# Kernel optimization log

Measured on AMD Instinct MI355X. Metric: run time of the kernel, lower is better.

## Reference

```python
import jax, jax.numpy as jnp
import numpy as np

V, H, L, NH, DH, FF, P, T = 21128, 768, 12, 12, 64, 3072, 512, 9
B, S = 16, 256
EPS = 1e-12

def _ln(x, g, b):
    m = x.mean(-1, keepdims=True)
    v = ((x - m) ** 2).mean(-1, keepdims=True)
    return (x - m) * jax.lax.rsqrt(v + EPS) * g + b

def setup_inputs() -> dict:
    key = jax.random.key(0)
    ks = iter(jax.random.split(key, 64))
    def nrm(shape, s=0.02):
        return (jax.random.normal(next(ks), shape, jnp.float32) * s)
    inp = {
        'input_ids': jax.random.randint(next(ks), (B, 1, S), 0, V, dtype=jnp.int32),
        'token_type_ids': jnp.zeros((B, 1, S), jnp.int32),
        'attention_mask': jnp.ones((B, 1, S), jnp.int32),
        'tags': jax.random.randint(next(ks), (B, S), 0, T, dtype=jnp.int32),
        'word_emb': nrm((V, H)), 'pos_emb': nrm((P, H)), 'type_emb': nrm((2, H)),
        'emb_ln_g': jnp.ones((H,), jnp.float32), 'emb_ln_b': jnp.zeros((H,), jnp.float32),
        'Wq': nrm((L, H, H)), 'bq': jnp.zeros((L, H), jnp.float32),
        'Wk': nrm((L, H, H)), 'bk': jnp.zeros((L, H), jnp.float32),
        'Wv': nrm((L, H, H)), 'bv': jnp.zeros((L, H), jnp.float32),
        'Wo': nrm((L, H, H)), 'bo': jnp.zeros((L, H), jnp.float32),
        'ln1_g': jnp.ones((L, H), jnp.float32), 'ln1_b': jnp.zeros((L, H), jnp.float32),
        'W1': nrm((L, H, FF)), 'b1': jnp.zeros((L, FF), jnp.float32),
        'W2': nrm((L, FF, H)), 'b2': jnp.zeros((L, H), jnp.float32),
        'ln2_g': jnp.ones((L, H), jnp.float32), 'ln2_b': jnp.zeros((L, H), jnp.float32),
        'dense_W': nrm((H, T)), 'dense_b': jnp.zeros((T,), jnp.float32),
        'crf_start': nrm((T,), 0.1), 'crf_end': nrm((T,), 0.1), 'crf_trans': nrm((T, T), 0.1),
    }
    return inp

def _model(input_ids, token_type_ids, attention_mask, tags,
           word_emb, pos_emb, type_emb, emb_ln_g, emb_ln_b,
           Wq, bq, Wk, bk, Wv, bv, Wo, bo, ln1_g, ln1_b,
           W1, b1, W2, b2, ln2_g, ln2_b, dense_W, dense_b,
           crf_start, crf_end, crf_trans):
    ids = input_ids[:, 0, :]            # [B,S]
    tt = token_type_ids[:, 0, :]
    amask = attention_mask[:, 0, :]     # [B,S] int
    Bn, Sn = ids.shape
    # --- BERT embeddings (post-LN BERT-base) ---
    x = word_emb[ids] + pos_emb[:Sn][None, :, :] + type_emb[tt]
    x = _ln(x, emb_ln_g, emb_ln_b)
    bias = jnp.where(amask[:, None, None, :] > 0, 0.0, -1e9).astype(x.dtype)  # [B,1,1,S]
    scale = 1.0 / np.sqrt(DH).astype(np.float32)
    def layer(h, p):
        wq, bq_, wk, bk_, wv, bv_, wo, bo_, g1, c1, w1, d1, w2, d2, g2, c2 = p
        q = (h @ wq + bq_).reshape(Bn, Sn, NH, DH).transpose(0, 2, 1, 3)
        k = (h @ wk + bk_).reshape(Bn, Sn, NH, DH).transpose(0, 2, 1, 3)
        v = (h @ wv + bv_).reshape(Bn, Sn, NH, DH).transpose(0, 2, 1, 3)
        att = jax.nn.softmax(jnp.einsum('bhqd,bhkd->bhqk', q, k) * scale + bias, axis=-1)
        ctx = jnp.einsum('bhqk,bhkd->bhqd', att, v).transpose(0, 2, 1, 3).reshape(Bn, Sn, H)
        h = _ln(h + ctx @ wo + bo_, g1, c1)
        ff = jax.nn.gelu(h @ w1 + d1, approximate=False)
        h = _ln(h + ff @ w2 + d2, g2, c2)
        return h, None
    x, _ = jax.lax.scan(layer, x, (Wq, bq, Wk, bk, Wv, bv, Wo, bo, ln1_g, ln1_b, W1, b1, W2, b2, ln2_g, ln2_b))
    # --- emission head, seq-first like the torch code ---
    emis = (x @ dense_W + dense_b).transpose(1, 0, 2)   # [S,B,T]
    m = (amask.T > 0)                                    # [S,B] bool
    tags_sb = tags.T                                     # [S,B]
    bidx = jnp.arange(Bn)
    # --- CRF numerator (gold path score) ---
    score0 = crf_start[tags_sb[0]] + emis[0, bidx, tags_sb[0]]
    def num_step(sc, inp):
        e, t, tp, mm = inp
        inc = crf_trans[tp, t] + e[bidx, t]
        return sc + jnp.where(mm, inc, 0.0), None
    score, _ = jax.lax.scan(num_step, score0, (emis[1:], tags_sb[1:], tags_sb[:-1], m[1:]))
    lengths = m.astype(jnp.int32).sum(0)                 # [B]
    last_tag = jnp.take_along_axis(tags_sb, (lengths - 1)[None, :], axis=0)[0]
    score = score + crf_end[last_tag]
    # --- CRF partition (forward algorithm) ---
    alpha0 = crf_start[None, :] + emis[0]                # [B,T]
    def fwd_step(a, inp):
        e, mm = inp
        nxt = jax.nn.logsumexp(a[:, :, None] + crf_trans[None, :, :] + e[:, None, :], axis=1)
        return jnp.where(mm[:, None], nxt, a), None
    alpha, _ = jax.lax.scan(fwd_step, alpha0, (emis[1:], m[1:]))
    logZ = jax.nn.logsumexp(alpha + crf_end[None, :], axis=-1)
    loss = -(score - logZ).mean()                        # reduction='mean'
    # --- Viterbi decode ---
    v0 = crf_start[None, :] + emis[0]
    tid = jnp.arange(T)
    def vit_step(vv, inp):
        e, mm = inp
        sc = vv[:, :, None] + crf_trans[None, :, :]       # [B,T,T]
        nv = sc.max(1) + e
        idx = sc.argmax(1).astype(jnp.int32)
        vv2 = jnp.where(mm[:, None], nv, vv)
        idx = jnp.where(mm[:, None], idx, tid[None, :].astype(jnp.int32))
        return vv2, idx
    vfin, hist = jax.lax.scan(vit_step, v0, (emis[1:], m[1:]))  # hist: [S-1,B,T]
    last = jnp.argmax(vfin + crf_end[None, :], axis=-1).astype(jnp.int32)  # [B]
    def back_step(t, h):
        prev = jnp.take_along_axis(h, t[:, None], axis=1)[:, 0]
        return prev, prev
    _, path = jax.lax.scan(back_step, last, hist, reverse=True)  # [S-1,B]
    preds = jnp.concatenate([path, last[None, :]], axis=0).T     # [B,S]
    return loss, preds

def reference(input_ids, token_type_ids, attention_mask, tags,
              word_emb, pos_emb, type_emb, emb_ln_g, emb_ln_b,
              Wq, bq, Wk, bk, Wv, bv, Wo, bo, ln1_g, ln1_b,
              W1, b1, W2, b2, ln2_g, ln2_b, dense_W, dense_b,
              crf_start, crf_end, crf_trans):
    return _model(input_ids, token_type_ids, attention_mask, tags,
                  word_emb, pos_emb, type_emb, emb_ln_g, emb_ln_b,
                  Wq, bq, Wk, bk, Wv, bv, Wo, bo, ln1_g, ln1_b,
                  W1, b1, W2, b2, ln2_g, ln2_b, dense_W, dense_b,
                  crf_start, crf_end, crf_trans)
```

## Files before the change

### kernel.cpp

```cpp
#include <hip/hip_runtime.h>
#include <math.h>

#define B_ 16
#define S_ 256
#define H_ 768
#define L_ 12
#define NH_ 12
#define DH_ 64
#define FF_ 3072
#define T_ 9

typedef unsigned short ushort_t;
typedef __attribute__((ext_vector_type(8))) __bf16 bf16x8;
typedef __attribute__((ext_vector_type(4))) float f32x4;
typedef __attribute__((ext_vector_type(4))) unsigned short us4;
typedef __attribute__((ext_vector_type(4))) unsigned int u32x4;

__device__ __forceinline__ ushort_t f2bf(float f) {
  union { float f; unsigned u; } v; v.f = f;
  unsigned r = v.u + 0x7FFFu + ((v.u >> 16) & 1u);
  return (ushort_t)(r >> 16);
}
__device__ __forceinline__ float bf2f(ushort_t h) {
  union { unsigned u; float f; } v; v.u = ((unsigned)h) << 16;
  return v.f;
}
__device__ __forceinline__ void gload16(const void* g, void* l) {
  __builtin_amdgcn_global_load_lds((const __attribute__((address_space(1))) void*)g,
                                   (__attribute__((address_space(3))) void*)l, 16, 0, 0);
}

__global__ __launch_bounds__(256) void emb_ln_kernel(const int* __restrict__ ids, const int* __restrict__ tt,
                              const float* __restrict__ we, const float* __restrict__ pe,
                              const float* __restrict__ te, const float* __restrict__ g,
                              const float* __restrict__ bb, float* __restrict__ out,
                              ushort_t* __restrict__ oh, ushort_t* __restrict__ ol) {
  const int token = blockIdx.x;
  const int tid = threadIdx.x;
  const int s = token & (S_ - 1);
  const int id = ids[token];
  const int t2 = tt[token];
  float x[3];
  float sum = 0.f;
#pragma unroll
  for (int i = 0; i < 3; ++i) {
    int d = tid + i * 256;
    x[i] = we[(size_t)id * H_ + d] + pe[(size_t)s * H_ + d] + te[(size_t)t2 * H_ + d];
    sum += x[i];
  }
  __shared__ float red[4];
#pragma unroll
  for (int o = 32; o > 0; o >>= 1) sum += __shfl_xor(sum, o, 64);
  const int wid = tid >> 6, lane = tid & 63;
  if (lane == 0) red[wid] = sum;
  __syncthreads();
  const float mean = (red[0] + red[1] + red[2] + red[3]) * (1.f / H_);
  float vs = 0.f;
#pragma unroll
  for (int i = 0; i < 3; ++i) { float dv = x[i] - mean; vs += dv * dv; }
#pragma unroll
  for (int o = 32; o > 0; o >>= 1) vs += __shfl_xor(vs, o, 64);
  __syncthreads();
  if (lane == 0) red[wid] = vs;
  __syncthreads();
  const float var = (red[0] + red[1] + red[2] + red[3]) * (1.f / H_);
  const float inv = rsqrtf(var + 1e-12f);
  float* op = out + (size_t)token * H_;
  ushort_t* hp = oh + (size_t)token * H_;
  ushort_t* lp = ol + (size_t)token * H_;
#pragma unroll
  for (int i = 0; i < 3; ++i) {
    int d = tid + i * 256;
    float y = (x[i] - mean) * inv * g[d] + bb[d];
    op[d] = y;
    ushort_t h = f2bf(y);
    hp[d] = h;
    lp[d] = f2bf(y - bf2f(h));
  }
}

__global__ __launch_bounds__(256) void ln_kernel(const float* __restrict__ base, const float* __restrict__ delta,
                          const float* __restrict__ g, const float* __restrict__ bb,
                          float* __restrict__ out, ushort_t* __restrict__ oh, ushort_t* __restrict__ ol) {
  const int token = blockIdx.x;
  const int tid = threadIdx.x;
  const float* bp = base + (size_t)token * H_;
  const float* dp = delta + (size_t)token * H_;
  float x[3];
  float s = 0.f;
#pragma unroll
  for (int i = 0; i < 3; ++i) { int d = tid + i * 256; x[i] = bp[d] + dp[d]; s += x[i]; }
  __shared__ float red[4];
#pragma unroll
  for (int o = 32; o > 0; o >>= 1) s += __shfl_xor(s, o, 64);
  const int wid = tid >> 6, lane = tid & 63;
  if (lane == 0) red[wid] = s;
  __syncthreads();
  const float mean = (red[0] + red[1] + red[2] + red[3]) * (1.f / H_);
  float vs = 0.f;
#pragma unroll
  for (int i = 0; i < 3; ++i) { float dv = x[i] - mean; vs += dv * dv; }
#pragma unroll
  for (int o = 32; o > 0; o >>= 1) vs += __shfl_xor(vs, o, 64);
  __syncthreads();
  if (lane == 0) red[wid] = vs;
  __syncthreads();
  const float var = (red[0] + red[1] + red[2] + red[3]) * (1.f / H_);
  const float inv = rsqrtf(var + 1e-12f);
  float* op = out + (size_t)token * H_;
  ushort_t* hp = oh + (size_t)token * H_;
  ushort_t* lp = ol + (size_t)token * H_;
#pragma unroll
  for (int i = 0; i < 3; ++i) {
    int d = tid + i * 256;
    float y = (x[i] - mean) * inv * g[d] + bb[d];
    op[d] = y;
    ushort_t h = f2bf(y);
    hp[d] = h;
    lp[d] = f2bf(y - bf2f(h));
  }
}

__device__ __forceinline__ void transpose_core(float (*t)[65], const float* __restrict__ src,
                                               ushort_t* __restrict__ dh,
                                               int K, int N, int n0, int k0) {
  const int tid = threadIdx.x;
#pragma unroll
  for (int i = 0; i < 16; ++i) {
    int lin = tid + i * 256;
    int kk = lin >> 6, nn = lin & 63;
    t[kk][nn] = src[(size_t)(k0 + kk) * N + n0 + nn];
  }
  __syncthreads();
#pragma unroll
  for (int i = 0; i < 16; ++i) {
    int lin = tid + i * 256;
    int nn = lin >> 6, kk = lin & 63;
    dh[(size_t)(n0 + nn) * K + k0 + kk] = f2bf(t[kk][nn]);
  }
}

__device__ __forceinline__ void wprep_dispatch(float (*t)[65], int wid,
                        const float* Wq, const float* Wk, const float* Wv, const float* Wo,
                        const float* W1, const float* W2,
                        ushort_t* WT4h, ushort_t* W1th, ushort_t* W2th) {
  if (wid < 576) {
    const int z = wid / 144, r = wid - z * 144;
    const int x = r % 12, y = r / 12;
    const float* src = z == 0 ? Wq : (z == 1 ? Wk : (z == 2 ? Wv : Wo));
    transpose_core(t, src, WT4h + (size_t)z * H_ * H_, H_, H_, x * 64, y * 64);
  } else if (wid < 1152) {
    const int i = wid - 576;
    const int x = i % 48, y = i / 48;
    transpose_core(t, W1, W1th, H_, FF_, x * 64, y * 64);
  } else {
    const int i = wid - 1152;
    const int x = i % 12, y = i / 12;
    transpose_core(t, W2, W2th, FF_, H_, x * 64, y * 64);
  }
}

__global__ __launch_bounds__(256) void wprep_k(const float* __restrict__ Wq, const float* __restrict__ Wk,
                        const float* __restrict__ Wv, const float* __restrict__ Wo,
                        const float* __restrict__ W1, const float* __restrict__ W2,
                        ushort_t* __restrict__ WT4h,
                        ushort_t* __restrict__ W1th, ushort_t* __restrict__ W2th) {
  __shared__ float t[64][65];
  wprep_dispatch(t, blockIdx.x, Wq, Wk, Wv, Wo, W1, W2, WT4h, W1th, W2th);
}

template <int R>
__device__ __forceinline__ void stage_slice(const ushort_t* __restrict__ gsrc, int K, char* lds) {
  const int tid = threadIdx.x;
  constexpr int NIT = (R * 4) / 256;
#pragma unroll
  for (int i = 0; i < NIT; ++i) {
    const int v = tid + i * 256;
    const int kh = v / (2 * R);
    const int r2 = v & (2 * R - 1);
    const int row = r2 >> 1;
    const int kg = (kh << 1) | ((r2 & 1) ^ ((row >> 2) & 1));
    gload16(gsrc + (size_t)row * K + kg * 8, lds + (i * 256 + (tid & 192)) * 16);
  }
}

template <int BM, int BN, int BK>
__device__ __forceinline__ void mgemm_acc(
    const ushort_t* __restrict__ Ah, const ushort_t* __restrict__ Al,
    const ushort_t* __restrict__ Bth,
    int K, f32x4 (&acc)[BM / 32][BN / 32], char* pool) {
  constexpr int FM = BM / 32;
  constexpr int FN = BN / 32;
  constexpr int ABYTES = BM * BK * 2;
  constexpr int BBYTES = BN * BK * 2;
  constexpr int BUF = 2 * ABYTES + BBYTES;
  const int tid = threadIdx.x;
  const int w = tid >> 6, lane = tid & 63;
  const int wm = w >> 1, wn = w & 1;
  const int kgL = lane >> 4, lr = lane & 15;
  const int row0 = blockIdx.y * BM, col0 = blockIdx.x * BN;

#pragma unroll
  for (int i = 0; i < FM; ++i)
#pragma unroll
    for (int j = 0; j < FN; ++j) acc[i][j] = (f32x4){0.f, 0.f, 0.f, 0.f};

  const int khL = kgL >> 1;
  const int swz = (((kgL & 1) ^ ((lr >> 2) & 1)) << 4);
  const int aB0 = khL * (BM * 32) + (wm * (BM / 2) + lr) * 32 + swz;
  const int bB0 = khL * (BN * 32) + (wn * (BN / 2) + lr) * 32 + swz;

  const ushort_t* gA_h = Ah + (size_t)row0 * K;
  const ushort_t* gA_l = Al + (size_t)row0 * K;
  const ushort_t* gB_h = Bth + (size_t)col0 * K;

  auto stageall = [&](int k0, char* buf) {
#pragma unroll
    for (int c = 0; c < BK / 32; ++c) {
      stage_slice<BM>(gA_h + k0 + c * 32, K, buf + c * BM * 64);
      stage_slice<BM>(gA_l + k0 + c * 32, K, buf + ABYTES + c * BM * 64);
      stage_slice<BN>(gB_h + k0 + c * 32, K, buf + 2 * ABYTES + c * BN * 64);
    }
  };

  const int nk = K / BK;
  stageall(0, pool);
  for (int k = 0; k < nk; ++k) {
    char* cur = pool + (k & 1) * BUF;
    if (k + 1 < nk) {
      stageall((k + 1) * BK, pool + ((k + 1) & 1) * BUF);
      asm volatile("s_waitcnt vmcnt(6)" ::: "memory");
    } else {
      asm volatile("s_waitcnt vmcnt(0)" ::: "memory");
    }
    __builtin_amdgcn_s_barrier();
    asm volatile("" ::: "memory");

#pragma unroll
    for (int ks = 0; ks < BK / 32; ++ks) {
      const char* aP = cur + ks * BM * 64;
      const char* bP = cur + 2 * ABYTES + ks * BN * 64;
      bf16x8 a_h[FM], a_l[FM], b_h[FN];
#pragma unroll
      for (int fm = 0; fm < FM; ++fm) {
        a_h[fm] = *(const bf16x8*)(aP + aB0 + fm * 512);
        a_l[fm] = *(const bf16x8*)(aP + ABYTES + aB0 + fm * 512);
      }
#pragma unroll
      for (int fn = 0; fn < FN; ++fn) {
        b_h[fn] = *(const bf16x8*)(bP + bB0 + fn * 512);
      }
#pragma unroll
      for (int fm = 0; fm < FM; ++fm)
#pragma unroll
        for (int fn = 0; fn < FN; ++fn) {
          f32x4 c = acc[fm][fn];
          c = __builtin_amdgcn_mfma_f32_16x16x32_bf16(a_h[fm], b_h[fn], c, 0, 0, 0);
          c = __builtin_amdgcn_mfma_f32_16x16x32_bf16(a_l[fm], b_h[fn], c, 0, 0, 0);
          acc[fm][fn] = c;
        }
    }
    asm volatile("" ::: "memory");
    __builtin_amdgcn_s_barrier();
  }
}

template <int BM, int BN, int BK, int EPI>
__global__ __launch_bounds__(256, 3) void mgemm(const ushort_t* __restrict__ Ah, const ushort_t* __restrict__ Al,
                      const ushort_t* __restrict__ Bth,
                      const float* __restrict__ bias, float* __restrict__ Cf,
                      ushort_t* __restrict__ Ch, ushort_t* __restrict__ Cl, int N, int K) {
  __shared__ __attribute__((aligned(16))) char pool[2 * (2 * BM * BK + BN * BK) * 2];
  f32x4 acc[BM / 32][BN / 32];
  mgemm_acc<BM, BN, BK>(Ah, Al, Bth, K, acc, pool);
  const int tid = threadIdx.x;
  const int w = tid >> 6, lane = tid & 63;
  const int wm = w >> 1, wn = w & 1;
  const int kg = lane >> 4, lr = lane & 15;
  const int row0 = blockIdx.y * BM, col0 = blockIdx.x * BN;
#pragma unroll
  for (int fn = 0; fn < BN / 32; ++fn) {
    const int col = col0 + wn * (BN / 2) + fn * 16 + lr;
    const float bv = bias[col];
#pragma unroll
    for (int fm = 0; fm < BM / 32; ++fm) {
#pragma unroll
      for (int r = 0; r < 4; ++r) {
        const int row = row0 + wm * (BM / 2) + fm * 16 + kg * 4 + r;
        float v = acc[fm][fn][r] + bv;
        if (EPI == 0) {
          Cf[(size_t)row * N + col] = v;
        } else {
          float gl = 0.5f * v * (1.f + erff(v * 0.70710678118654752f));
          ushort_t h = f2bf(gl);
          Ch[(size_t)row * N + col] = h;
          Cl[(size_t)row * N + col] = f2bf(gl - bf2f(h));
        }
      }
    }
  }
}

__global__ __launch_bounds__(256, 3) void ff1_fused(
    const ushort_t* __restrict__ Xh, const ushort_t* __restrict__ Xl,
    const ushort_t* __restrict__ W1th, const float* __restrict__ bias,
    ushort_t* __restrict__ Ch, ushort_t* __restrict__ Cl,
    const float* __restrict__ WqN, const float* __restrict__ WkN,
    const float* __restrict__ WvN, const float* __restrict__ WoN,
    const float* __restrict__ W1N, const float* __restrict__ W2N,
    ushort_t* __restrict__ WT4hN, ushort_t* __restrict__ W1thN, ushort_t* __restrict__ W2thN) {
  __shared__ __attribute__((aligned(16))) char pool[49152];
  if (blockIdx.y >= 32) {
    if (WqN == nullptr) return;
    const int wid = (blockIdx.y - 32) * 24 + blockIdx.x;
    wprep_dispatch((float(*)[65])pool, wid, WqN, WkN, WvN, WoN, W1N, W2N, WT4hN, W1thN, W2thN);
    return;
  }
  f32x4 acc[4][4];
  mgemm_acc<128, 128, 32>(Xh, Xl, W1th, H_, acc, pool);
  const int tid = threadIdx.x;
  const int w = tid >> 6, lane = tid & 63;
  const int wm = w >> 1, wn = w & 1;
  const int kg = lane >> 4, lr = lane & 15;
  const int row0 = blockIdx.y * 128, col0 = blockIdx.x * 128;
#pragma unroll
  for (int fn = 0; fn < 4; ++fn) {
    const int col = col0 + wn * 64 + fn * 16 + lr;
    const float bv = bias[col];
#pragma unroll
    for (int fm = 0; fm < 4; ++fm) {
#pragma unroll
      for (int r = 0; r < 4; ++r) {
        const int row = row0 + wm * 64 + fm * 16 + kg * 4 + r;
        float v = acc[fm][fn][r] + bv;
        float gl = 0.5f * v * (1.f + erff(v * 0.70710678118654752f));
        ushort_t h = f2bf(gl);
        Ch[(size_t)row * FF_ + col] = h;
        Cl[(size_t)row * FF_ + col] = f2bf(gl - bf2f(h));
      }
    }
  }
}

__global__ __launch_bounds__(256, 3) void qkv_m(const ushort_t* __restrict__ Xh, const ushort_t* __restrict__ Xl,
                      const ushort_t* __restrict__ WT4h,
                      const float* __restrict__ bq, const float* __restrict__ bk,
                      const float* __restrict__ bvv,
                      ushort_t* __restrict__ Qh, ushort_t* __restrict__ Ql,
                      ushort_t* __restrict__ Kh, ushort_t* __restrict__ Vth) {
  __shared__ __attribute__((aligned(16))) char pool[49152];
  const int z = blockIdx.z;
  const ushort_t* Bh = WT4h + (size_t)z * H_ * H_;
  const float* bias = z == 0 ? bq : (z == 1 ? bk : bvv);
  f32x4 acc[4][4];
  mgemm_acc<128, 128, 32>(Xh, Xl, Bh, H_, acc, pool);
  const int tid = threadIdx.x;
  const int w = tid >> 6, lane = tid & 63;
  const int wm = w >> 1, wn = w & 1;
  const int kg = lane >> 4, lr = lane & 15;
  const int row0 = blockIdx.y * 128, col0 = blockIdx.x * 128;
#pragma unroll
  for (int fn = 0; fn < 4; ++fn) {
    const int col = col0 + wn * 64 + fn * 16 + lr;
    const float bv = bias[col];
#pragma unroll
    for (int fm = 0; fm < 4; ++fm) {
      const int rowb = row0 + wm * 64 + fm * 16 + kg * 4;
      if (z == 0) {
#pragma unroll
        for (int r = 0; r < 4; ++r) {
          float v = acc[fm][fn][r] + bv;
          ushort_t h = f2bf(v);
          Qh[(size_t)(rowb + r) * H_ + col] = h;
          Ql[(size_t)(rowb + r) * H_ + col] = f2bf(v - bf2f(h));
        }
      } else if (z == 1) {
#pragma unroll
        for (int r = 0; r < 4; ++r) {
          Kh[(size_t)(rowb + r) * H_ + col] = f2bf(acc[fm][fn][r] + bv);
        }
      } else {
        us4 h4;
#pragma unroll
        for (int r = 0; r < 4; ++r) h4[r] = f2bf(acc[fm][fn][r] + bv);
        const int bb2 = rowb >> 8, s0 = rowb & 255;
        const int hh2 = col >> 6, d = col & 63;
        *(us4*)(Vth + ((size_t)(bb2 * NH_ + hh2) * DH_ + d) * S_ + s0) = h4;
      }
    }
  }
}

__global__ __launch_bounds__(256, 3) void attn_mfma(
    const ushort_t* __restrict__ Qh, const ushort_t* __restrict__ Ql,
    const ushort_t* __restrict__ Kh, const ushort_t* __restrict__ Vth,
    const int* __restrict__ amask,
    ushort_t* __restrict__ Oh, ushort_t* __restrict__ Ol) {
  const int bid = blockIdx.x;
  const int qt = bid / 192;
  const int gh = bid - qt * 192;
  const int b = gh / NH_;
  const int h = gh - b * NH_;
  __shared__ __attribute__((aligned(16))) ushort_t sKh[2][64 * 64];
  __shared__ __attribute__((aligned(16))) ushort_t sVh[2][64 * 64];
  __shared__ __attribute__((aligned(16))) unsigned sP[4][16 * 68];
  __shared__ float sBias[2][64];
  const int tid = threadIdx.x;
  const int w = tid >> 6, lane = tid & 63;
  const int kg = lane >> 4, lr = lane & 15;

  const int qrow = b * S_ + qt * 64 + w * 16 + lr;
  bf16x8 qfh[2], qfl[2];
#pragma unroll
  for (int ds2 = 0; ds2 < 2; ++ds2) {
    const size_t off = (size_t)qrow * H_ + h * DH_ + ds2 * 32 + kg * 8;
    qfh[ds2] = *(const bf16x8*)(Qh + off);
    qfl[ds2] = *(const bf16x8*)(Ql + off);
  }

  f32x4 ctx[4];
#pragma unroll
  for (int i = 0; i < 4; ++i) ctx[i] = (f32x4){0.f, 0.f, 0.f, 0.f};
  float mrow[4], lrw[4];
#pragma unroll
  for (int r = 0; r < 4; ++r) { mrow[r] = -1e30f; lrw[r] = 0.f; }

  unsigned* sPw = &sP[w][0];

  auto stageKV = [&](int kt, int bufi) {
#pragma unroll
    for (int i = 0; i < 2; ++i) {
      const int v = tid + i * 256;
      const int row = v >> 3;
      const int c16 = (v & 7) ^ (row & 7);
      const size_t kgl = (size_t)(b * S_ + kt * 64 + row) * H_ + h * DH_ + c16 * 8;
      gload16(Kh + kgl, (char*)&sKh[bufi][0] + v * 16);
      const size_t vgl = (size_t)((b * NH_ + h) * DH_ + row) * S_ + kt * 64 + c16 * 8;
      gload16(Vth + vgl, (char*)&sVh[bufi][0] + v * 16);
    }
    if (tid < 64) sBias[bufi][tid] = (amask[b * S_ + kt * 64 + tid] > 0) ? 0.f : -1e9f;
  };

  stageKV(0, 0);
  for (int kt = 0; kt < 4; ++kt) {
    const int bi = kt & 1;
    if (kt < 3) {
      stageKV(kt + 1, bi ^ 1);
      asm volatile("s_waitcnt vmcnt(4) lgkmcnt(0)" ::: "memory");
    } else {
      asm volatile("s_waitcnt vmcnt(0) lgkmcnt(0)" ::: "memory");
    }
    __builtin_amdgcn_s_barrier();
    asm volatile("" ::: "memory");

    f32x4 sc[4];
#pragma unroll
    for (int kf = 0; kf < 4; ++kf) sc[kf] = (f32x4){0.f, 0.f, 0.f, 0.f};
#pragma unroll
    for (int kf = 0; kf < 4; ++kf) {
      const int krow = kf * 16 + lr;
#pragma unroll
      for (int ds2 = 0; ds2 < 2; ++ds2) {
        const int cb = (ds2 * 64 + kg * 16) ^ ((krow & 7) << 4);
        const bf16x8 kvh = *(const bf16x8*)((const char*)&sKh[bi][0] + krow * 128 + cb);
        sc[kf] = __builtin_amdgcn_mfma_f32_16x16x32_bf16(qfh[ds2], kvh, sc[kf], 0, 0, 0);
        sc[kf] = __builtin_amdgcn_mfma_f32_16x16x32_bf16(qfl[ds2], kvh, sc[kf], 0, 0, 0);
      }
    }
    float bsv[4];
#pragma unroll
    for (int kf = 0; kf < 4; ++kf) bsv[kf] = sBias[bi][kf * 16 + lr];

#pragma unroll
    for (int r = 0; r < 4; ++r) {
      float sv[4];
      float tmax = -1e30f;
#pragma unroll
      for (int kf = 0; kf < 4; ++kf) {
        sv[kf] = sc[kf][r] * 0.125f + bsv[kf];
        tmax = fmaxf(tmax, sv[kf]);
      }
#pragma unroll
      for (int o = 8; o > 0; o >>= 1) tmax = fmaxf(tmax, __shfl_xor(tmax, o, 64));
      const float mnew = fmaxf(mrow[r], tmax);
      const float corr = expf(mrow[r] - mnew);
      float ls = 0.f;
      const int qoff = (kg * 4 + r) * 68;
#pragma unroll
      for (int kf = 0; kf < 4; ++kf) {
        const float pe = expf(sv[kf] - mnew);
        ls += pe;
        const ushort_t hi = f2bf(pe);
        const ushort_t lo = f2bf(pe - bf2f(hi));
        sPw[qoff + kf * 16 + lr] = ((unsigned)hi << 16) | lo;
      }
#pragma unroll
      for (int o = 8; o > 0; o >>= 1) ls += __shfl_xor(ls, o, 64);
      lrw[r] = lrw[r] * corr + ls;
      mrow[r] = mnew;
#pragma unroll
      for (int df = 0; df < 4; ++df) ctx[df][r] *= corr;
    }

#pragma unroll
    for (int ks = 0; ks < 2; ++ks) {
      unsigned w8[8];
      *(u32x4*)&w8[0] = *(const u32x4*)(sPw + lr * 68 + ks * 32 + kg * 8);
      *(u32x4*)&w8[4] = *(const u32x4*)(sPw + lr * 68 + ks * 32 + kg * 8 + 4);
      union { bf16x8 v; ushort_t u[8]; } ph, pl;
#pragma unroll
      for (int j = 0; j < 8; ++j) { ph.u[j] = (ushort_t)(w8[j] >> 16); pl.u[j] = (ushort_t)(w8[j] & 0xffffu); }
#pragma unroll
      for (int df = 0; df < 4; ++df) {
        const int vrow = df * 16 + lr;
        const int cb = (ks * 64 + kg * 16) ^ ((vrow & 7) << 4);
        const bf16x8 vvh = *(const bf16x8*)((const char*)&sVh[bi][0] + vrow * 128 + cb);
        ctx[df] = __builtin_amdgcn_mfma_f32_16x16x32_bf16(ph.v, vvh, ctx[df], 0, 0, 0);
        ctx[df] = __builtin_amdgcn_mfma_f32_16x16x32_bf16(pl.v, vvh, ctx[df], 0, 0, 0);
      }
    }
    asm volatile("" ::: "memory");
    __builtin_amdgcn_s_barrier();
  }

#pragma unroll
  for (int r = 0; r < 4; ++r) {
    const float inv = 1.f / lrw[r];
    const int tok = b * S_ + qt * 64 + w * 16 + kg * 4 + r;
#pragma unroll
    for (int df = 0; df < 4; ++df) {
      const float v = ctx[df][r] * inv;
      const ushort_t hi = f2bf(v);
      const size_t o = (size_t)tok * H_ + h * DH_ + df * 16 + lr;
      Oh[o] = hi;
      Ol[o] = f2bf(v - bf2f(hi));
    }
  }
}

__global__ __launch_bounds__(256) void emis_kernel(const float* __restrict__ X, const float* __restrict__ W,
                            const float* __restrict__ bias, float* __restrict__ E) {
  const int wave = (blockIdx.x * 256 + threadIdx.x) >> 6;
  const int lane = threadIdx.x & 63;
  const int b = wave >> 8, s = wave & 255;
  const float* xp = X + (size_t)wave * H_;
  float acc[T_];
#pragma unroll
  for (int t = 0; t < T_; ++t) acc[t] = 0.f;
  for (int i = 0; i < 12; ++i) {
    const int d = lane + i * 64;
    const float xv = xp[d];
    const float* wp = W + (size_t)d * T_;
#pragma unroll
    for (int t = 0; t < T_; ++t) acc[t] = fmaf(xv, wp[t], acc[t]);
  }
#pragma unroll
  for (int t = 0; t < T_; ++t) {
    float v = acc[t];
#pragma unroll
    for (int o = 32; o > 0; o >>= 1) v += __shfl_xor(v, o, 64);
    acc[t] = v;
  }
  if (lane < T_) E[((size_t)s * B_ + b) * T_ + lane] = acc[lane] + bias[lane];
}

__global__ __launch_bounds__(128) void crf_kernel(const float* __restrict__ emis, const int* __restrict__ tags,
                          const int* __restrict__ amask,
                          const float* __restrict__ crf_start, const float* __restrict__ crf_end,
                          const float* __restrict__ trans,
                          float* __restrict__ partial, float* __restrict__ out) {
  const int b = blockIdx.x;
  const int tid = threadIdx.x;
  const int wv = tid >> 6;
  const int lane = tid & 63;
  __shared__ float sE[S_ * T_];
  __shared__ float sM[S_];
  __shared__ float trs[T_ * T_];
  __shared__ unsigned char hist[S_ - 1][16];
  __shared__ float pathf[S_];
  for (int i = tid; i < S_ * T_; i += 128) {
    const int s = i / T_, t = i - s * T_;
    sE[i] = emis[((size_t)s * B_ + b) * T_ + t];
  }
  for (int i = tid; i < S_; i += 128) sM[i] = (float)amask[b * S_ + i];
  for (int i = tid; i < T_ * T_; i += 128) trs[i] = trans[i];
  __syncthreads();

  const int t = lane;
  const bool act = t < T_;
  float trc[T_];
#pragma unroll
  for (int p = 0; p < T_; ++p) trc[p] = act ? trs[p * T_ + t] : 0.f;

  if (wv == 0) {
    float alpha = act ? crf_start[t] + sE[t] : 0.f;
    for (int s = 1; s < S_; ++s) {
      float ap[T_];
#pragma unroll
      for (int p = 0; p < T_; ++p) ap[p] = __shfl(alpha, p, 64);
      if (act) {
        const float e = sE[s * T_ + t];
        float mx = -1e30f;
#pragma unroll
        for (int p = 0; p < T_; ++p) mx = fmaxf(mx, ap[p] + trc[p]);
        float sum = 0.f;
#pragma unroll
        for (int p = 0; p < T_; ++p) sum += __expf(ap[p] + trc[p] - mx);
        const float na = mx + __logf(sum) + e;
        if (sM[s] > 0.f) alpha = na;
      }
    }
    float nsum = 0.f;
    int len = 0;
#pragma unroll
    for (int j = 0; j < 4; ++j) {
      const int s = lane + j * 64;
      const int mk = (sM[s] > 0.f) ? 1 : 0;
      len += mk;
      if (s >= 1 && mk) {
        const int tc = tags[b * S_ + s], tp = tags[b * S_ + s - 1];
        nsum += trs[tp * T_ + tc] + sE[s * T_ + tc];
      }
    }
#pragma unroll
    for (int o = 32; o > 0; o >>= 1) {
      nsum += __shfl_xor(nsum, o, 64);
      len += __shfl_xor(len, o, 64);
    }
    const float fz = act ? alpha + crf_end[t] : -1e30f;
    float zp[T_];
#pragma unroll
    for (int p = 0; p < T_; ++p) zp[p] = __shfl(fz, p, 64);
    if (lane == 0) {
      float mx = -1e30f;
#pragma unroll
      for (int p = 0; p < T_; ++p) mx = fmaxf(mx, zp[p]);
      float sum = 0.f;
#pragma unroll
      for (int p = 0; p < T_; ++p) sum += __expf(zp[p] - mx);
      const float logZ = mx + __logf(sum);
      const int tg0 = tags[b * S_];
      const float score = nsum + crf_start[tg0] + sE[tg0] + crf_end[tags[b * S_ + len - 1]];
      partial[b] = score - logZ;
    }
  } else {
    float vit = act ? crf_start[t] + sE[t] : 0.f;
    for (int s = 1; s < S_; ++s) {
      float vp[T_];
#pragma unroll
      for (int p = 0; p < T_; ++p) vp[p] = __shfl(vit, p, 64);
      if (act) {
        const float e = sE[s * T_ + t];
        float best = -1e30f; int bi = 0;
#pragma unroll
        for (int p = 0; p < T_; ++p) {
          const float scv = vp[p] + trc[p];
          if (scv > best) { best = scv; bi = p; }
        }
        if (sM[s] > 0.f) {
          vit = best + e;
          hist[s - 1][t] = (unsigned char)bi;
        } else {
          hist[s - 1][t] = (unsigned char)t;
        }
      }
    }
    const float fv = act ? vit + crf_end[t] : -1e30f;
    float wp[T_];
#pragma unroll
    for (int p = 0; p < T_; ++p) wp[p] = __shfl(fv, p, 64);
    if (lane == 0) {
      float best = -1e30f; int lastTag = 0;
#pragma unroll
      for (int p = 0; p < T_; ++p) {
        if (wp[p] > best) { best = wp[p]; lastTag = p; }
      }
      int tc = lastTag;
      pathf[S_ - 1] = (float)tc;
      for (int i = S_ - 2; i >= 0; --i) {
        tc = hist[i][tc];
        pathf[i] = (float)tc;
      }
    }
  }
  __syncthreads();
#pragma unroll
  for (int j = 0; j < 2; ++j) {
    const int s = tid + j * 128;
    out[1 + b * S_ + s] = pathf[s];
  }
}

__global__ __launch_bounds__(64) void crf_final(const float* __restrict__ partial, float* __restrict__ out) {
  const int lane = threadIdx.x;
  float v = (lane < B_) ? partial[lane] : 0.f;
#pragma unroll
  for (int o = 32; o > 0; o >>= 1) v += __shfl_xor(v, o, 64);
  if (lane == 0) out[0] = -(v * (1.f / B_));
}

extern "C" void kernel_launch(void* const* d_in, const int* in_sizes, int n_in,
                              void* d_out, int out_size, void* d_ws, size_t ws_size,
                              hipStream_t stream) {
  const int* input_ids = (const int*)d_in[0];
  const int* token_type_ids = (const int*)d_in[1];
  const int* attention_mask = (const int*)d_in[2];
  const int* tags = (const int*)d_in[3];
  const float* word_emb = (const float*)d_in[4];
  const float* pos_emb = (const float*)d_in[5];
  const float* type_emb = (const float*)d_in[6];
  const float* emb_ln_g = (const float*)d_in[7];
  const float* emb_ln_b = (const float*)d_in[8];
  const float* Wq = (const float*)d_in[9];
  const float* bq = (const float*)d_in[10];
  const float* Wk = (const float*)d_in[11];
  const float* bk = (const float*)d_in[12];
  const float* Wv = (const float*)d_in[13];
  const float* bv = (const float*)d_in[14];
  const float* Wo = (const float*)d_in[15];
  const float* bo = (const float*)d_in[16];
  const float* ln1_g = (const float*)d_in[17];
  const float* ln1_b = (const float*)d_in[18];
  const float* W1 = (const float*)d_in[19];
  const float* b1 = (const float*)d_in[20];
  const float* W2 = (const float*)d_in[21];
  const float* b2 = (const float*)d_in[22];
  const float* ln2_g = (const float*)d_in[23];
  const float* ln2_b = (const float*)d_in[24];
  const float* dense_W = (const float*)d_in[25];
  const float* dense_b = (const float*)d_in[26];
  const float* crf_start = (const float*)d_in[27];
  const float* crf_end = (const float*)d_in[28];
  const float* crf_trans = (const float*)d_in[29];

  constexpr size_t NTOK = (size_t)B_ * S_;
  constexpr size_t XSZ = NTOK * H_;
  constexpr size_t WT4SZ = (size_t)4 * H_ * H_;
  constexpr size_t WFSZ = (size_t)H_ * FF_;

  char* p = (char*)d_ws;
  float* X = (float*)p;            p += XSZ * 4;
  float* TMP = (float*)p;          p += XSZ * 4;
  char* UN = p;                    p += 8 * XSZ * 2;
  ushort_t* Qh = (ushort_t*)UN;
  ushort_t* Ql = Qh + XSZ;
  ushort_t* Kh = Ql + XSZ;
  ushort_t* Vth = Kh + XSZ;
  ushort_t* CTXh = Vth + XSZ;
  ushort_t* CTXl = CTXh + XSZ;
  ushort_t* FFh = (ushort_t*)UN;
  ushort_t* FFl = FFh + NTOK * FF_;
  ushort_t* Xh = (ushort_t*)p;     p += XSZ * 2;
  ushort_t* Xl = (ushort_t*)p;     p += XSZ * 2;
  ushort_t* WT4h2 = (ushort_t*)p;  p += WT4SZ * 2 * 2;
  ushort_t* W1th2 = (ushort_t*)p;  p += WFSZ * 2 * 2;
  ushort_t* W2th2 = (ushort_t*)p;  p += WFSZ * 2 * 2;
  float* EM = (float*)p;           p += (size_t)S_ * B_ * T_ * 4;
  float* PART = (float*)p;         p += B_ * 4;

  emb_ln_kernel<<<dim3(4096), dim3(256), 0, stream>>>(input_ids, token_type_ids, word_emb, pos_emb,
                                                      type_emb, emb_ln_g, emb_ln_b, X, Xh, Xl);
  wprep_k<<<dim3(1728), dim3(256), 0, stream>>>(Wq, Wk, Wv, Wo, W1, W2, WT4h2, W1th2, W2th2);

  for (int l = 0; l < L_; ++l) {
    const int pr = l & 1, pn = (l + 1) & 1;
    ushort_t* WT4h = WT4h2 + (size_t)pr * WT4SZ;
    ushort_t* W1th = W1th2 + (size_t)pr * WFSZ;
    ushort_t* W2th = W2th2 + (size_t)pr * WFSZ;
    const bool hasNext = (l + 1 < L_);
    const size_t wo_n = (size_t)(l + 1) * H_ * H_;

    qkv_m<<<dim3(6, 32, 3), dim3(256), 0, stream>>>(Xh, Xl, WT4h, bq + (size_t)l * H_,
                                                    bk + (size_t)l * H_, bv + (size_t)l * H_,
                                                    Qh, Ql, Kh, Vth);
    attn_mfma<<<dim3(768), dim3(256), 0, stream>>>(Qh, Ql, Kh, Vth, attention_mask, CTXh, CTXl);
    mgemm<64, 64, 64, 0><<<dim3(12, 64), dim3(256), 0, stream>>>(
        CTXh, CTXl, WT4h + (size_t)3 * H_ * H_,
        bo + (size_t)l * H_, TMP, nullptr, nullptr, H_, H_);
    ln_kernel<<<dim3(4096), dim3(256), 0, stream>>>(X, TMP, ln1_g + (size_t)l * H_,
                                                    ln1_b + (size_t)l * H_, X, Xh, Xl);
    ff1_fused<<<dim3(24, 32 + 72), dim3(256), 0, stream>>>(
        Xh, Xl, W1th, b1 + (size_t)l * FF_, FFh, FFl,
        hasNext ? Wq + wo_n : nullptr, Wk + wo_n, Wv + wo_n, Wo + wo_n,
        W1 + (size_t)(l + 1) * WFSZ, W2 + (size_t)(l + 1) * WFSZ,
        WT4h2 + (size_t)pn * WT4SZ, W1th2 + (size_t)pn * WFSZ, W2th2 + (size_t)pn * WFSZ);
    mgemm<64, 64, 64, 0><<<dim3(12, 64), dim3(256), 0, stream>>>(
        FFh, FFl, W2th, b2 + (size_t)l * H_, TMP, nullptr, nullptr, H_, FF_);
    ln_kernel<<<dim3(4096), dim3(256), 0, stream>>>(X, TMP, ln2_g + (size_t)l * H_,
                                                    ln2_b + (size_t)l * H_, X, Xh, Xl);
  }

  emis_kernel<<<dim3(1024), dim3(256), 0, stream>>>(X, dense_W, dense_b, EM);
  crf_kernel<<<dim3(B_), dim3(128), 0, stream>>>(EM, tags, attention_mask, crf_start, crf_end,
                                                 crf_trans, PART, (float*)d_out);
  crf_final<<<dim3(1), dim3(64), 0, stream>>>(PART, (float*)d_out);
}
```

Measured before the change: 3.385 ms.

## Fuse Q/K/V projections into one block sharing A tiles; enlarge out-proj/FF2 tiles

The QKV kernel now computes all three projections in one block. Each block stages the shared activation hi/lo slices once alongside three weight slices in a double-buffered LDS pipeline, instead of launching three z-slices that each reload the activations. The output-projection and FF2 GEMMs switch from 64x64x64 to 128x128x32 tiles with a quarter as many blocks. Both changes raise reuse per loaded tile. In exchange there are more accumulator registers (48 f32x4), the occupancy hint is dropped, and the grids are much smaller (192 blocks), which may underfill the GPU's CUs.

Result: faster. 3.163 ms (-6.6%).

```diff
diff --git a/kernel.cpp b/kernel.cpp
--- a/kernel.cpp
+++ b/kernel.cpp
@@ -342,47 +342,110 @@
   }
 }
 
-__global__ __launch_bounds__(256, 3) void qkv_m(const ushort_t* __restrict__ Xh, const ushort_t* __restrict__ Xl,
+__global__ __launch_bounds__(256) void qkv_m(const ushort_t* __restrict__ Xh, const ushort_t* __restrict__ Xl,
                       const ushort_t* __restrict__ WT4h,
                       const float* __restrict__ bq, const float* __restrict__ bk,
                       const float* __restrict__ bvv,
                       ushort_t* __restrict__ Qh, ushort_t* __restrict__ Ql,
                       ushort_t* __restrict__ Kh, ushort_t* __restrict__ Vth) {
-  __shared__ __attribute__((aligned(16))) char pool[49152];
-  const int z = blockIdx.z;
-  const ushort_t* Bh = WT4h + (size_t)z * H_ * H_;
-  const float* bias = z == 0 ? bq : (z == 1 ? bk : bvv);
-  f32x4 acc[4][4];
-  mgemm_acc<128, 128, 32>(Xh, Xl, Bh, H_, acc, pool);
+  constexpr int ABYTES = 128 * 32 * 2;
+  constexpr int BUF = 2 * ABYTES + 3 * ABYTES;
+  __shared__ __attribute__((aligned(16))) char pool[2 * BUF];
   const int tid = threadIdx.x;
   const int w = tid >> 6, lane = tid & 63;
   const int wm = w >> 1, wn = w & 1;
-  const int kg = lane >> 4, lr = lane & 15;
+  const int kgL = lane >> 4, lr = lane & 15;
   const int row0 = blockIdx.y * 128, col0 = blockIdx.x * 128;
+
+  f32x4 acc[3][4][4];
+#pragma unroll
+  for (int z = 0; z < 3; ++z)
+#pragma unroll
+    for (int i = 0; i < 4; ++i)
+#pragma unroll
+      for (int j = 0; j < 4; ++j) acc[z][i][j] = (f32x4){0.f, 0.f, 0.f, 0.f};
+
+  const int khL = kgL >> 1;
+  const int swz = (((kgL & 1) ^ ((lr >> 2) & 1)) << 4);
+  const int aB0 = khL * (128 * 32) + (wm * 64 + lr) * 32 + swz;
+  const int bB0 = khL * (128 * 32) + (wn * 64 + lr) * 32 + swz;
+
+  const ushort_t* gA_h = Xh + (size_t)row0 * H_;
+  const ushort_t* gA_l = Xl + (size_t)row0 * H_;
+  const ushort_t* gB0 = WT4h + (size_t)col0 * H_;
+  const ushort_t* gB1 = WT4h + (size_t)H_ * H_ + (size_t)col0 * H_;
+  const ushort_t* gB2 = WT4h + (size_t)2 * H_ * H_ + (size_t)col0 * H_;
+
+  auto stageall = [&](int k0, char* buf) {
+    stage_slice<128>(gA_h + k0, H_, buf);
+    stage_slice<128>(gA_l + k0, H_, buf + ABYTES);
+    stage_slice<128>(gB0 + k0, H_, buf + 2 * ABYTES);
+    stage_slice<128>(gB1 + k0, H_, buf + 3 * ABYTES);
+    stage_slice<128>(gB2 + k0, H_, buf + 4 * ABYTES);
+  };
+
+  const int nk = H_ / 32;
+  stageall(0, pool);
+  for (int k = 0; k < nk; ++k) {
+    char* cur = pool + (k & 1) * BUF;
+    if (k + 1 < nk) {
+      stageall((k + 1) * 32, pool + ((k + 1) & 1) * BUF);
+      asm volatile("s_waitcnt vmcnt(10)" ::: "memory");
+    } else {
+      asm volatile("s_waitcnt vmcnt(0)" ::: "memory");
+    }
+    __builtin_amdgcn_s_barrier();
+    asm volatile("" ::: "memory");
+
+    bf16x8 a_h[4], a_l[4];
+#pragma unroll
+    for (int fm = 0; fm < 4; ++fm) {
+      a_h[fm] = *(const bf16x8*)(cur + aB0 + fm * 512);
+      a_l[fm] = *(const bf16x8*)(cur + ABYTES + aB0 + fm * 512);
+    }
+#pragma unroll
+    for (int z = 0; z < 3; ++z) {
+      const char* bP = cur + (2 + z) * ABYTES;
+      bf16x8 b_h[4];
+#pragma unroll
+      for (int fn = 0; fn < 4; ++fn) b_h[fn] = *(const bf16x8*)(bP + bB0 + fn * 512);
+#pragma unroll
+      for (int fm = 0; fm < 4; ++fm)
+#pragma unroll
+        for (int fn = 0; fn < 4; ++fn) {
+          f32x4 c = acc[z][fm][fn];
+          c = __builtin_amdgcn_mfma_f32_16x16x32_bf16(a_h[fm], b_h[fn], c, 0, 0, 0);
+          c = __builtin_amdgcn_mfma_f32_16x16x32_bf16(a_l[fm], b_h[fn], c, 0, 0, 0);
+          acc[z][fm][fn] = c;
+        }
+    }
+    asm volatile("" ::: "memory");
+    __builtin_amdgcn_s_barrier();
+  }
+
+  const int kg = kgL;
 #pragma unroll
   for (int fn = 0; fn < 4; ++fn) {
     const int col = col0 + wn * 64 + fn * 16 + lr;
-    const float bv = bias[col];
+    const float bvq = bq[col], bvk = bk[col], bvv2 = bvv[col];
 #pragma unroll
     for (int fm = 0; fm < 4; ++fm) {
       const int rowb = row0 + wm * 64 + fm * 16 + kg * 4;
-      if (z == 0) {
-#pragma unroll
-        for (int r = 0; r < 4; ++r) {
-          float v = acc[fm][fn][r] + bv;
-          ushort_t h = f2bf(v);
-          Qh[(size_t)(rowb + r) * H_ + col] = h;
-          Ql[(size_t)(rowb + r) * H_ + col] = f2bf(v - bf2f(h));
-        }
-      } else if (z == 1) {
-#pragma unroll
-        for (int r = 0; r < 4; ++r) {
-          Kh[(size_t)(rowb + r) * H_ + col] = f2bf(acc[fm][fn][r] + bv);
-        }
-      } else {
+#pragma unroll
+      for (int r = 0; r < 4; ++r) {
+        float v = acc[0][fm][fn][r] + bvq;
+        ushort_t h = f2bf(v);
+        Qh[(size_t)(rowb + r) * H_ + col] = h;
+        Ql[(size_t)(rowb + r) * H_ + col] = f2bf(v - bf2f(h));
+      }
+#pragma unroll
+      for (int r = 0; r < 4; ++r) {
+        Kh[(size_t)(rowb + r) * H_ + col] = f2bf(acc[1][fm][fn][r] + bvk);
+      }
+      {
         us4 h4;
 #pragma unroll
-        for (int r = 0; r < 4; ++r) h4[r] = f2bf(acc[fm][fn][r] + bv);
+        for (int r = 0; r < 4; ++r) h4[r] = f2bf(acc[2][fm][fn][r] + bvv2);
         const int bb2 = rowb >> 8, s0 = rowb & 255;
         const int hh2 = col >> 6, d = col & 63;
         *(us4*)(Vth + ((size_t)(bb2 * NH_ + hh2) * DH_ + d) * S_ + s0) = h4;
@@ -770,11 +833,11 @@
     const bool hasNext = (l + 1 < L_);
     const size_t wo_n = (size_t)(l + 1) * H_ * H_;
 
-    qkv_m<<<dim3(6, 32, 3), dim3(256), 0, stream>>>(Xh, Xl, WT4h, bq + (size_t)l * H_,
-                                                    bk + (size_t)l * H_, bv + (size_t)l * H_,
-                                                    Qh, Ql, Kh, Vth);
+    qkv_m<<<dim3(6, 32), dim3(256), 0, stream>>>(Xh, Xl, WT4h, bq + (size_t)l * H_,
+                                                 bk + (size_t)l * H_, bv + (size_t)l * H_,
+                                                 Qh, Ql, Kh, Vth);
     attn_mfma<<<dim3(768), dim3(256), 0, stream>>>(Qh, Ql, Kh, Vth, attention_mask, CTXh, CTXl);
-    mgemm<64, 64, 64, 0><<<dim3(12, 64), dim3(256), 0, stream>>>(
+    mgemm<128, 128, 32, 0><<<dim3(6, 32), dim3(256), 0, stream>>>(
         CTXh, CTXl, WT4h + (size_t)3 * H_ * H_,
         bo + (size_t)l * H_, TMP, nullptr, nullptr, H_, H_);
     ln_kernel<<<dim3(4096), dim3(256), 0, stream>>>(X, TMP, ln1_g + (size_t)l * H_,
@@ -784,7 +847,7 @@
         hasNext ? Wq + wo_n : nullptr, Wk + wo_n, Wv + wo_n, Wo + wo_n,
         W1 + (size_t)(l + 1) * WFSZ, W2 + (size_t)(l + 1) * WFSZ,
         WT4h2 + (size_t)pn * WT4SZ, W1th2 + (size_t)pn * WFSZ, W2th2 + (size_t)pn * WFSZ);
-    mgemm<64, 64, 64, 0><<<dim3(12, 64), dim3(256), 0, stream>>>(
+    mgemm<128, 128, 32, 0><<<dim3(6, 32), dim3(256), 0, stream>>>(
         FFh, FFl, W2th, b2 + (size_t)l * H_, TMP, nullptr, nullptr, H_, FF_);
     ln_kernel<<<dim3(4096), dim3(256), 0, stream>>>(X, TMP, ln2_g + (size_t)l * H_,
                                                     ln2_b + (size_t)l * H_, X, Xh, Xl);
```
